# Kernel optimization log

Hardware: AMD Instinct MI355X
Metric: run time of the kernel (lower is better)

Reference implementation:

```python
import jax, jax.numpy as jnp
import numpy as np

DIM = 4096
N_HEADS = 32
N_KV_HEADS = 8
HEAD_DIM = 128
WINDOW = 1024
SEQ = 2048
ROPE_THETA = 10000.0


def setup_inputs() -> dict:
    key = jax.random.key(0)
    ks = jax.random.split(key, 5)
    x = jax.random.normal(ks[0], (SEQ, DIM), dtype=jnp.float32)
    # torch nn.Linear weights are [out_features, in_features]
    wq = jax.random.normal(ks[1], (N_HEADS * HEAD_DIM, DIM), dtype=jnp.float32) * (DIM ** -0.5)
    wk = jax.random.normal(ks[2], (N_KV_HEADS * HEAD_DIM, DIM), dtype=jnp.float32) * (DIM ** -0.5)
    wv = jax.random.normal(ks[3], (N_KV_HEADS * HEAD_DIM, DIM), dtype=jnp.float32) * (DIM ** -0.5)
    wo = jax.random.normal(ks[4], (DIM, N_HEADS * HEAD_DIM), dtype=jnp.float32) * ((N_HEADS * HEAD_DIM) ** -0.5)
    # RoPE freqs: freqs_cis[t, i] = exp(1j * t * theta^(-2i/d)); store cos/sin
    inv_freq = ROPE_THETA ** (-jnp.arange(0, HEAD_DIM, 2, dtype=jnp.float32) / HEAD_DIM)  # [D/2]
    angles = jnp.arange(SEQ, dtype=jnp.float32)[:, None] * inv_freq[None, :]  # [S, D/2]
    return {"x": x, "wq": wq, "wk": wk, "wv": wv, "wo": wo,
            "cos": jnp.cos(angles), "sin": jnp.sin(angles)}


def _apply_rope(t, cos, sin):
    # t: [S, H, D]; cos/sin: [S, D/2] -> rotate consecutive pairs as complex mul
    S, H, D = t.shape
    tr = t.reshape(S, H, D // 2, 2)
    t0, t1 = tr[..., 0], tr[..., 1]
    c = cos[:, None, :]
    s = sin[:, None, :]
    out = jnp.stack([t0 * c - t1 * s, t0 * s + t1 * c], axis=-1)
    return out.reshape(S, H, D)


def reference(x, wq, wk, wv, wo, cos, sin):
    S = x.shape[0]
    repeats = N_HEADS // N_KV_HEADS
    scale = HEAD_DIM ** -0.5
    q = (x @ wq.T).reshape(S, N_HEADS, HEAD_DIM)
    k = (x @ wk.T).reshape(S, N_KV_HEADS, HEAD_DIM)
    v = (x @ wv.T).reshape(S, N_KV_HEADS, HEAD_DIM)
    q = _apply_rope(q, cos, sin)
    k = _apply_rope(k, cos, sin)
    # repeat_kv: repeat_interleave along head axis (GQA)
    k = jnp.repeat(k, repeats, axis=1)  # [S, H, D]
    v = jnp.repeat(v, repeats, axis=1)
    scores = jnp.einsum('qhd,khd->hqk', q, k) * scale  # [H, S, S]
    # sliding-window causal mask: attend to j in (i - WINDOW, i]
    i = jnp.arange(S)[:, None]
    j = jnp.arange(S)[None, :]
    allowed = (j <= i) & (i - j < WINDOW)  # [S, S]
    scores = jnp.where(allowed[None, :, :], scores, jnp.finfo(scores.dtype).min)
    probs = jax.nn.softmax(scores, axis=-1)
    out = jnp.einsum('hqk,khd->qhd', probs, v).reshape(S, N_HEADS * HEAD_DIM)
    return out @ wo.T
```

## Files before the change

### kernel.cpp

```cpp
#include <hip/hip_runtime.h>

#define DIM 4096
#define NH 32
#define NKV 8
#define HD 128
#define WINDOW 1024
#define SEQ 2048
#define QLD 6144

typedef unsigned int uint32;
typedef __attribute__((ext_vector_type(8))) short short8_t;
typedef __attribute__((ext_vector_type(8))) __bf16 bf16x8_t;
typedef __attribute__((ext_vector_type(4))) float floatx4_t;

__device__ __forceinline__ uint32 f2bf_bits(float f) {
  uint32 u = __builtin_bit_cast(uint32, f);
  return (u + 0x7fffu + ((u >> 16) & 1u)) >> 16;
}
__device__ __forceinline__ float bf2f(unsigned short b) {
  return __builtin_bit_cast(float, ((uint32)b) << 16);
}

template <class X, class Y> struct same_t { static constexpr bool v = false; };
template <class X> struct same_t<X, X> { static constexpr bool v = true; };

__device__ __forceinline__ void load_lds16(const unsigned short* g, unsigned short* l) {
  __builtin_amdgcn_global_load_lds((__attribute__((address_space(1))) void*)g,
                                   (__attribute__((address_space(3))) void*)l, 16, 0, 0);
}

template <typename TC, bool ROPE, int JT>
__global__ __launch_bounds__(256, 2) void gemm_bf16(const unsigned short* __restrict__ A,
                                                    const unsigned short* __restrict__ B,
                                                    TC* __restrict__ C,
                                                    int M, int N, int K,
                                                    const float* __restrict__ cosp,
                                                    const float* __restrict__ sinp,
                                                    int rope_ncols) {
  constexpr int BN = 32 * JT;
  constexpr int WN = 16 * JT;
  __shared__ unsigned short As[128 * 64];
  __shared__ unsigned short Bs[BN * 64];
  const int tid = threadIdx.x;
  const int lane = tid & 63, w = tid >> 6;
  const int quad = lane >> 4, l16 = lane & 15;
  const int wm = w >> 1, wn = w & 1;
  const size_t m0 = (size_t)blockIdx.y * 128, n0 = (size_t)blockIdx.x * BN;

  const int srow = tid >> 3;
  const int scol = ((tid & 7) ^ (srow & 7)) << 3;
  const unsigned short* Abase = A + (m0 + srow) * (size_t)K + scol;
  const unsigned short* Bbase = B + (n0 + srow) * (size_t)K + scol;
  unsigned short* ldsA = As + (tid >> 6) * 512;
  unsigned short* ldsB = Bs + (tid >> 6) * 512;

  const int sa = l16 & 7;
  const int raA = wm * 64 + l16;
  const int raB = wn * WN + l16;

  floatx4_t acc[4][JT] = {};

  const int nk = K >> 6;
  for (int kt = 0; kt < nk; kt++) {
    const int kbase = kt << 6;
#pragma unroll
    for (int i = 0; i < 4; i++)
      load_lds16(Abase + kbase + (size_t)(i * 32) * K, ldsA + i * 2048);
#pragma unroll
    for (int i = 0; i < JT; i++)
      load_lds16(Bbase + kbase + (size_t)(i * 32) * K, ldsB + i * 2048);
    __syncthreads();
#pragma unroll
    for (int ks = 0; ks < 2; ks++) {
      bf16x8_t af[4], bfg[JT];
#pragma unroll
      for (int i = 0; i < 4; i++) {
        const int colA = (((ks << 2) | quad) ^ sa) << 3;
        af[i] = __builtin_bit_cast(bf16x8_t,
            *(const short8_t*)(&As[(raA + i * 16) * 64 + colA]));
      }
#pragma unroll
      for (int j = 0; j < JT; j++) {
        const int colB = (((ks << 2) | quad) ^ sa) << 3;
        bfg[j] = __builtin_bit_cast(bf16x8_t,
            *(const short8_t*)(&Bs[(raB + j * 16) * 64 + colB]));
      }
#pragma unroll
      for (int i = 0; i < 4; i++)
#pragma unroll
        for (int j = 0; j < JT; j++)
          acc[i][j] = __builtin_amdgcn_mfma_f32_16x16x32_bf16(af[i], bfg[j], acc[i][j], 0, 0, 0);
    }
    __syncthreads();
  }
#pragma unroll
  for (int i = 0; i < 4; i++)
#pragma unroll
    for (int j = 0; j < JT; j++) {
      const int colb = (int)n0 + wn * WN + j * 16;
      const bool do_rope = ROPE && (colb < rope_ncols);
#pragma unroll
      for (int r = 0; r < 4; r++) {
        size_t row = m0 + wm * 64 + i * 16 + quad * 4 + r;
        size_t col = n0 + wn * WN + j * 16 + l16;
        float v = acc[i][j][r];
        if constexpr (ROPE) {
          if (do_rope) {
            float pv = __shfl_xor(v, 1);
            const int d = ((int)col & 127) >> 1;
            const float c = cosp[row * 64 + d];
            const float s = sinp[row * 64 + d];
            v = ((int)col & 1) ? (pv * s + v * c) : (v * c - pv * s);
          }
        }
        if constexpr (same_t<TC, float>::v)
          C[row * (size_t)N + col] = v;
        else
          C[row * (size_t)N + col] = (unsigned short)f2bf_bits(v);
      }
    }
}

__global__ __launch_bounds__(256) void cvt4_kernel(const float* __restrict__ s0,
                                                   const float* __restrict__ s1,
                                                   const float* __restrict__ s2,
                                                   const float* __restrict__ s3,
                                                   unsigned short* __restrict__ d0,
                                                   unsigned short* __restrict__ d1,
                                                   unsigned short* __restrict__ d2,
                                                   unsigned short* __restrict__ d3) {
  const int b = blockIdx.x;
  const float* src;
  unsigned short* dst;
  int rb;
  if (b < 4096)        { src = s0; dst = d0; rb = b; }
  else if (b < 12288)  { src = s1; dst = d1; rb = b - 4096; }
  else if (b < 14336)  { src = s2; dst = d2; rb = b - 12288; }
  else                 { src = s3; dst = d3; rb = b - 14336; }
  const int idx = rb * 256 + threadIdx.x;
  const float4* p = (const float4*)src + (size_t)idx * 2;
  float4 a = p[0], bb = p[1];
  uint32 w0 = f2bf_bits(a.x) | (f2bf_bits(a.y) << 16);
  uint32 w1 = f2bf_bits(a.z) | (f2bf_bits(a.w) << 16);
  uint32 w2 = f2bf_bits(bb.x) | (f2bf_bits(bb.y) << 16);
  uint32 w3 = f2bf_bits(bb.z) | (f2bf_bits(bb.w) << 16);
  ((uint4*)dst)[idx] = make_uint4(w0, w1, w2, w3);
}

__global__ __launch_bounds__(256) void epi_kernel(const float* __restrict__ wo,
                                                  unsigned short* __restrict__ wob,
                                                  const unsigned short* __restrict__ v,
                                                  unsigned short* __restrict__ vT) {
  __shared__ unsigned short t[64][72];
  const int b = blockIdx.x;
  const int tid = threadIdx.x;
  if (b < 8192) {
    const int idx = b * 256 + tid;
    const float4* p = (const float4*)wo + (size_t)idx * 2;
    float4 a = p[0], bb = p[1];
    uint32 w0 = f2bf_bits(a.x) | (f2bf_bits(a.y) << 16);
    uint32 w1 = f2bf_bits(a.z) | (f2bf_bits(a.w) << 16);
    uint32 w2 = f2bf_bits(bb.x) | (f2bf_bits(bb.y) << 16);
    uint32 w3 = f2bf_bits(bb.z) | (f2bf_bits(bb.w) << 16);
    ((uint4*)wob)[idx] = make_uint4(w0, w1, w2, w3);
    return;
  }
  const int bx = b - 8192;
  const int r0 = (bx & 15) * 64, s0 = (bx >> 4) * 64;
#pragma unroll
  for (int it = 0; it < 2; it++) {
    int f = it * 256 + tid;
    int si = f >> 3, cj = (f & 7) << 3;
    *(short8_t*)(&t[si][cj]) = *(const short8_t*)(v + (size_t)(s0 + si) * QLD + r0 + cj);
  }
  __syncthreads();
#pragma unroll
  for (int it = 0; it < 2; it++) {
    int f = it * 256 + tid;
    int ri = f >> 3, sj = (f & 7) << 3;
    short8_t o;
#pragma unroll
    for (int jj = 0; jj < 8; jj++) o[jj] = t[sj + jj][ri];
    *(short8_t*)(vT + (size_t)(r0 + ri) * SEQ + s0 + sj) = o;
  }
}

__global__ __launch_bounds__(512, 4) void attn_kernel(const unsigned short* __restrict__ qb,
                                                      const unsigned short* __restrict__ kb,
                                                      const unsigned short* __restrict__ vT,
                                                      unsigned short* __restrict__ attn_out) {
  const int h = blockIdx.x;
  const int qt = 15 - blockIdx.y;
  const int kvh = h >> 2;
  const int q0 = qt * 128;
  const int tid = threadIdx.x;
  const int w = tid >> 6, lane = tid & 63;
  const int quad = lane >> 4, l16 = lane & 15;
  const float SCALE = 0.08838834764831845f;

  __shared__ unsigned short Ks[64 * 128];
  __shared__ unsigned short VTs[128 * 64];
  __shared__ unsigned short PTs[8 * 16 * 72];

  unsigned short* pt = &PTs[w * 1152];

  const int krow = tid >> 4;
  const int kc16 = tid & 15;
  const int kgcol = (kc16 ^ (krow & 7)) << 3;
  const unsigned short* kgbase = kb + (size_t)krow * QLD + kvh * 128 + kgcol;
  const int vrow = tid >> 3;
  const int vc8 = tid & 7;
  const int vgcol = (vc8 ^ (vrow & 7)) << 3;
  const unsigned short* vgbase = vT + (size_t)(kvh * 128 + vrow) * 2048 + vgcol;
  unsigned short* ldsK = Ks + w * 512;
  unsigned short* ldsV = VTs + w * 512;

  bf16x8_t aq[4];
  {
    const unsigned short* qp = qb + (size_t)(q0 + w * 16 + l16) * QLD + h * 128 + quad * 8;
#pragma unroll
    for (int ks = 0; ks < 4; ks++)
      aq[ks] = __builtin_bit_cast(bf16x8_t, *(const short8_t*)(qp + ks * 32));
  }

  floatx4_t O[8] = {};
  float m_run[4], l_run[4];
#pragma unroll
  for (int r = 0; r < 4; r++) { m_run[r] = -3e38f; l_run[r] = 0.0f; }

  const int qmin = q0 + w * 16, qmax = qmin + 15;
  int kbeg = q0 - (WINDOW - 1); if (kbeg < 0) kbeg = 0;
  const int c0 = kbeg & ~63;
  const int nch = (q0 + 128 - c0) >> 6;
  const int sa = l16 & 7;

  for (int ci = 0; ci < nch; ci++) {
    const int kb0 = c0 + (ci << 6);
#pragma unroll
    for (int i = 0; i < 2; i++)
      load_lds16(kgbase + (size_t)(kb0 + i * 32) * QLD, ldsK + i * 4096);
#pragma unroll
    for (int i = 0; i < 2; i++)
      load_lds16(vgbase + kb0 + (size_t)(i * 64) * 2048, ldsV + i * 4096);
    __syncthreads();
    const bool alive = (kb0 <= qmax) && (kb0 + 63 >= qmin - (WINDOW - 1));
    if (alive) {
      floatx4_t S[4];
      __builtin_amdgcn_s_setprio(1);
#pragma unroll
      for (int j = 0; j < 4; j++) {
        floatx4_t acc = {};
        const int keyrow = j * 16 + l16;
#pragma unroll
        for (int ks = 0; ks < 4; ks++) {
          const int c16 = ((ks << 2) | quad) ^ sa;
          bf16x8_t bfk = __builtin_bit_cast(bf16x8_t,
              *(const short8_t*)(&Ks[keyrow * 128 + c16 * 8]));
          acc = __builtin_amdgcn_mfma_f32_16x16x32_bf16(aq[ks], bfk, acc, 0, 0, 0);
        }
        S[j] = acc;
      }
      __builtin_amdgcn_s_setprio(0);
      const bool need_mask = (kb0 + 63 > qmin) || (qmax - kb0 >= WINDOW);
      if (need_mask) {
#pragma unroll
        for (int j = 0; j < 4; j++) {
          const int key = kb0 + j * 16 + l16;
#pragma unroll
          for (int r = 0; r < 4; r++) {
            const int i = qmin + quad * 4 + r;
            const bool ok = (key <= i) && (i - key < WINDOW);
            S[j][r] = ok ? S[j][r] : -3e38f;
          }
        }
      }
      float mx[4], rs[4], alpha[4];
#pragma unroll
      for (int r = 0; r < 4; r++) {
        float m = S[0][r];
#pragma unroll
        for (int j = 1; j < 4; j++) m = fmaxf(m, S[j][r]);
#pragma unroll
        for (int d = 1; d < 16; d <<= 1) m = fmaxf(m, __shfl_xor(m, d, 16));
        mx[r] = fmaxf(m_run[r], m);
        alpha[r] = __expf(SCALE * (m_run[r] - mx[r]));
        m_run[r] = mx[r];
        rs[r] = 0.0f;
      }
#pragma unroll
      for (int j = 0; j < 4; j++) {
        float p[4];
#pragma unroll
        for (int r = 0; r < 4; r++) {
          const float sv = S[j][r];
          float e = __expf(SCALE * (sv - mx[r]));
          if (need_mask) e = (sv < -1e37f) ? 0.0f : e;
          p[r] = e;
          rs[r] += e;
        }
#pragma unroll
        for (int r = 0; r < 4; r++)
          pt[(quad * 4 + r) * 72 + j * 16 + l16] = (unsigned short)f2bf_bits(p[r]);
      }
#pragma unroll
      for (int r = 0; r < 4; r++) {
#pragma unroll
        for (int d = 1; d < 16; d <<= 1) rs[r] += __shfl_xor(rs[r], d, 16);
        l_run[r] = l_run[r] * alpha[r] + rs[r];
      }
#pragma unroll
      for (int nt = 0; nt < 8; nt++)
#pragma unroll
        for (int r = 0; r < 4; r++) O[nt][r] *= alpha[r];
      asm volatile("" ::: "memory");
      __builtin_amdgcn_s_setprio(1);
#pragma unroll
      for (int ks = 0; ks < 2; ks++) {
        bf16x8_t af = __builtin_bit_cast(bf16x8_t,
            *(const short8_t*)(&pt[l16 * 72 + ks * 32 + quad * 8]));
#pragma unroll
        for (int nt = 0; nt < 8; nt++) {
          const int c8 = (((ks << 2) | quad) ^ sa);
          bf16x8_t bfv = __builtin_bit_cast(bf16x8_t,
              *(const short8_t*)(&VTs[(nt * 16 + l16) * 64 + c8 * 8]));
          O[nt] = __builtin_amdgcn_mfma_f32_16x16x32_bf16(af, bfv, O[nt], 0, 0, 0);
        }
      }
      __builtin_amdgcn_s_setprio(0);
    }
    __syncthreads();
  }
  float inv_l[4];
#pragma unroll
  for (int r = 0; r < 4; r++) inv_l[r] = 1.0f / l_run[r];
#pragma unroll
  for (int nt = 0; nt < 8; nt++)
#pragma unroll
    for (int r = 0; r < 4; r++) {
      float v = O[nt][r] * inv_l[r];
      attn_out[(size_t)(qmin + quad * 4 + r) * 4096 + h * 128 + nt * 16 + l16] =
          (unsigned short)f2bf_bits(v);
    }
}

extern "C" void kernel_launch(void* const* d_in, const int* in_sizes, int n_in,
                              void* d_out, int out_size, void* d_ws, size_t ws_size,
                              hipStream_t stream) {
  (void)in_sizes; (void)n_in; (void)out_size; (void)ws_size;
  const float* x    = (const float*)d_in[0];
  const float* wq   = (const float*)d_in[1];
  const float* wk   = (const float*)d_in[2];
  const float* wv   = (const float*)d_in[3];
  const float* wo   = (const float*)d_in[4];
  const float* cosp = (const float*)d_in[5];
  const float* sinp = (const float*)d_in[6];
  float* out = (float*)d_out;
  char* ws = (char*)d_ws;

  unsigned short* wqkvb = (unsigned short*)(ws);
  unsigned short* wob   = (unsigned short*)(ws);
  unsigned short* vTb   = (unsigned short*)(ws + 33554432);
  unsigned short* xb    = (unsigned short*)(ws + 50331648);
  unsigned short* attnb = (unsigned short*)(ws + 50331648);
  unsigned short* qkvb  = (unsigned short*)(ws + 67108864);

  cvt4_kernel<<<16384, 256, 0, stream>>>(
      x, wq, wk, wv,
      xb, wqkvb, wqkvb + (size_t)4096 * 4096, wqkvb + (size_t)5120 * 4096);
  gemm_bf16<unsigned short, true, 6><<<dim3(32, 16), 256, 0, stream>>>(
      xb, wqkvb, qkvb, SEQ, QLD, DIM, cosp, sinp, 5120);
  epi_kernel<<<8704, 256, 0, stream>>>(wo, wob, qkvb + 5120, vTb);
  attn_kernel<<<dim3(NH, 16), 512, 0, stream>>>(qkvb, qkvb + 4096, vTb, attnb);
  gemm_bf16<float, false, 4><<<dim3(32, 16), 256, 0, stream>>>(
      attnb, wob, out, SEQ, 4096, DIM, nullptr, nullptr, 0);
}
```

Baseline: 465.0 us.

## Replace GEMM with triple-buffered pipelined kernel using larger tiles

Replaces the single-buffered bf16 GEMM with a 512-thread kernel. It uses a three-stage LDS ring with BK=32, where global-to-LDS loads for tile t+2 are issued while tile t is computed, gated by explicit vmcnt waits and raw s_barrier. Block tiles are enlarged (256x192 for QKV, 128x256 for the output projection), the LDS swizzle changes, and setprio is raised around the MFMA block. This aims to hide global memory latency and improve data reuse, at the cost of hand-tuned waitcnt correctness risk, higher LDS and register use, and fewer blocks (256) on a large-CU device.

```diff
diff --git a/kernel.cpp b/kernel.cpp
--- a/kernel.cpp
+++ b/kernel.cpp
@@ -29,80 +29,118 @@
                                    (__attribute__((address_space(3))) void*)l, 16, 0, 0);
 }
 
-template <typename TC, bool ROPE, int JT>
-__global__ __launch_bounds__(256, 2) void gemm_bf16(const unsigned short* __restrict__ A,
+template <typename TC, bool ROPE, int BM, int BN>
+__global__ __launch_bounds__(512, 2) void gemm_pipe(const unsigned short* __restrict__ A,
                                                     const unsigned short* __restrict__ B,
-                                                    TC* __restrict__ C,
-                                                    int M, int N, int K,
+                                                    TC* __restrict__ C, int N, int K,
                                                     const float* __restrict__ cosp,
                                                     const float* __restrict__ sinp,
                                                     int rope_ncols) {
-  constexpr int BN = 32 * JT;
-  constexpr int WN = 16 * JT;
-  __shared__ unsigned short As[128 * 64];
-  __shared__ unsigned short Bs[BN * 64];
+  constexpr int BK = 32;
+  constexpr int MI = BM / 32;
+  constexpr int NJ = BN / 64;
+  constexpr int IA = (BM * 64) / 8192;
+  constexpr int IT = IA + 2;
+  constexpr int AE = BM * BK;
+  constexpr int BUFE = 14336;
+  __shared__ unsigned short lds[3 * BUFE];
+
   const int tid = threadIdx.x;
-  const int lane = tid & 63, w = tid >> 6;
+  const int w = tid >> 6, lane = tid & 63;
   const int quad = lane >> 4, l16 = lane & 15;
-  const int wm = w >> 1, wn = w & 1;
-  const size_t m0 = (size_t)blockIdx.y * 128, n0 = (size_t)blockIdx.x * BN;
-
-  const int srow = tid >> 3;
-  const int scol = ((tid & 7) ^ (srow & 7)) << 3;
-  const unsigned short* Abase = A + (m0 + srow) * (size_t)K + scol;
-  const unsigned short* Bbase = B + (n0 + srow) * (size_t)K + scol;
-  unsigned short* ldsA = As + (tid >> 6) * 512;
-  unsigned short* ldsB = Bs + (tid >> 6) * 512;
-
-  const int sa = l16 & 7;
-  const int raA = wm * 64 + l16;
-  const int raB = wn * WN + l16;
-
-  floatx4_t acc[4][JT] = {};
-
-  const int nk = K >> 6;
-  for (int kt = 0; kt < nk; kt++) {
-    const int kbase = kt << 6;
-#pragma unroll
-    for (int i = 0; i < 4; i++)
-      load_lds16(Abase + kbase + (size_t)(i * 32) * K, ldsA + i * 2048);
-#pragma unroll
-    for (int i = 0; i < JT; i++)
-      load_lds16(Bbase + kbase + (size_t)(i * 32) * K, ldsB + i * 2048);
-    __syncthreads();
-#pragma unroll
-    for (int ks = 0; ks < 2; ks++) {
-      bf16x8_t af[4], bfg[JT];
-#pragma unroll
-      for (int i = 0; i < 4; i++) {
-        const int colA = (((ks << 2) | quad) ^ sa) << 3;
-        af[i] = __builtin_bit_cast(bf16x8_t,
-            *(const short8_t*)(&As[(raA + i * 16) * 64 + colA]));
-      }
-#pragma unroll
-      for (int j = 0; j < JT; j++) {
-        const int colB = (((ks << 2) | quad) ^ sa) << 3;
-        bfg[j] = __builtin_bit_cast(bf16x8_t,
-            *(const short8_t*)(&Bs[(raB + j * 16) * 64 + colB]));
-      }
-#pragma unroll
-      for (int i = 0; i < 4; i++)
-#pragma unroll
-        for (int j = 0; j < JT; j++)
-          acc[i][j] = __builtin_amdgcn_mfma_f32_16x16x32_bf16(af[i], bfg[j], acc[i][j], 0, 0, 0);
+  const int wm = w >> 2, wn = w & 3;
+  const size_t m0 = (size_t)blockIdx.y * BM, n0 = (size_t)blockIdx.x * BN;
+
+  const unsigned short* asrc[IA];
+  const unsigned short* bsrc[2];
+#pragma unroll
+  for (int ii = 0; ii < IA; ii++) {
+    const int rloc = ii * 128 + (tid >> 2);
+    const int c = ((tid & 3) + 4 - ((rloc >> 1) & 3)) & 3;
+    asrc[ii] = A + (m0 + rloc) * (size_t)K + c * 8;
+  }
+#pragma unroll
+  for (int ii = 0; ii < 2; ii++) {
+    const int r0 = ii ? (BN - 128) : 0;
+    const int rloc = r0 + (tid >> 2);
+    const int c = ((tid & 3) + 4 - ((rloc >> 1) & 3)) & 3;
+    bsrc[ii] = B + (n0 + rloc) * (size_t)K + c * 8;
+  }
+  const int bdst1 = AE + (BN - 128) * BK;
+
+  int aoff[MI], boff[NJ];
+#pragma unroll
+  for (int i = 0; i < MI; i++) {
+    const int row = wm * (BM / 2) + i * 16 + l16;
+    const int s = (quad + (row >> 1)) & 3;
+    aoff[i] = row * BK + s * 8;
+  }
+#pragma unroll
+  for (int j = 0; j < NJ; j++) {
+    const int row = wn * (BN / 4) + j * 16 + l16;
+    const int s = (quad + (row >> 1)) & 3;
+    boff[j] = AE + row * BK + s * 8;
+  }
+
+  auto stage = [&](int kt, int bi) {
+    unsigned short* buf = lds + bi * BUFE + w * 512;
+    const size_t ko = (size_t)kt * BK;
+#pragma unroll
+    for (int ii = 0; ii < IA; ii++)
+      load_lds16(asrc[ii] + ko, buf + ii * 4096);
+    load_lds16(bsrc[0] + ko, buf + AE);
+    load_lds16(bsrc[1] + ko, buf + bdst1);
+  };
+
+  floatx4_t acc[MI][NJ] = {};
+  const int nt = K >> 5;
+
+  stage(0, 0);
+  stage(1, 1);
+  int rb = 0;
+  for (int t = 0; t < nt; t++) {
+    int sb = rb + 2; if (sb >= 3) sb -= 3;
+    if (t + 2 < nt) {
+      stage(t + 2, sb);
+      if constexpr (IT == 4) asm volatile("s_waitcnt vmcnt(8)" ::: "memory");
+      else                   asm volatile("s_waitcnt vmcnt(6)" ::: "memory");
+    } else if (t + 2 == nt) {
+      if constexpr (IT == 4) asm volatile("s_waitcnt vmcnt(4)" ::: "memory");
+      else                   asm volatile("s_waitcnt vmcnt(3)" ::: "memory");
+    } else {
+      asm volatile("s_waitcnt vmcnt(0)" ::: "memory");
     }
-    __syncthreads();
-  }
-#pragma unroll
-  for (int i = 0; i < 4; i++)
-#pragma unroll
-    for (int j = 0; j < JT; j++) {
-      const int colb = (int)n0 + wn * WN + j * 16;
+    __builtin_amdgcn_s_barrier();
+    const unsigned short* buf = lds + rb * BUFE;
+    bf16x8_t afr[MI], bfr[NJ];
+#pragma unroll
+    for (int i = 0; i < MI; i++)
+      afr[i] = __builtin_bit_cast(bf16x8_t, *(const short8_t*)(buf + aoff[i]));
+#pragma unroll
+    for (int j = 0; j < NJ; j++)
+      bfr[j] = __builtin_bit_cast(bf16x8_t, *(const short8_t*)(buf + boff[j]));
+    asm volatile("s_waitcnt lgkmcnt(0)" ::: "memory");
+    __builtin_amdgcn_s_barrier();
+    __builtin_amdgcn_s_setprio(1);
+#pragma unroll
+    for (int i = 0; i < MI; i++)
+#pragma unroll
+      for (int j = 0; j < NJ; j++)
+        acc[i][j] = __builtin_amdgcn_mfma_f32_16x16x32_bf16(afr[i], bfr[j], acc[i][j], 0, 0, 0);
+    __builtin_amdgcn_s_setprio(0);
+    rb = (rb == 2) ? 0 : rb + 1;
+  }
+
+#pragma unroll
+  for (int i = 0; i < MI; i++)
+#pragma unroll
+    for (int j = 0; j < NJ; j++) {
+      const int colb = (int)n0 + wn * (BN / 4) + j * 16;
       const bool do_rope = ROPE && (colb < rope_ncols);
 #pragma unroll
       for (int r = 0; r < 4; r++) {
-        size_t row = m0 + wm * 64 + i * 16 + quad * 4 + r;
-        size_t col = n0 + wn * WN + j * 16 + l16;
+        size_t row = m0 + wm * (BM / 2) + i * 16 + quad * 4 + r;
+        size_t col = n0 + wn * (BN / 4) + j * 16 + l16;
         float v = acc[i][j][r];
         if constexpr (ROPE) {
           if (do_rope) {
@@ -367,10 +405,10 @@
   cvt4_kernel<<<16384, 256, 0, stream>>>(
       x, wq, wk, wv,
       xb, wqkvb, wqkvb + (size_t)4096 * 4096, wqkvb + (size_t)5120 * 4096);
-  gemm_bf16<unsigned short, true, 6><<<dim3(32, 16), 256, 0, stream>>>(
-      xb, wqkvb, qkvb, SEQ, QLD, DIM, cosp, sinp, 5120);
+  gemm_pipe<unsigned short, true, 256, 192><<<dim3(32, 8), 512, 0, stream>>>(
+      xb, wqkvb, qkvb, QLD, DIM, cosp, sinp, 5120);
   epi_kernel<<<8704, 256, 0, stream>>>(wo, wob, qkvb + 5120, vTb);
   attn_kernel<<<dim3(NH, 16), 512, 0, stream>>>(qkvb, qkvb + 4096, vTb, attnb);
-  gemm_bf16<float, false, 4><<<dim3(32, 16), 256, 0, stream>>>(
-      attnb, wob, out, SEQ, 4096, DIM, nullptr, nullptr, 0);
-}
+  gemm_pipe<float, false, 128, 256><<<dim3(16, 16), 512, 0, stream>>>(
+      attnb, wob, out, 4096, DIM, nullptr, nullptr, 0);
+}
```

New measurement: 477.2 us. +2.6%, slower.
